# Optimization experiments

Measured on AMD Instinct MI355X. Metric: run time of the kernel, lower is better.

Reference implementation:

```python
import jax, jax.numpy as jnp
import numpy as np
from jax import lax

CONF_THR = 0.5
NMS_THR = 0.5
B, N, C = 2, 8192, 80


def setup_inputs() -> dict:
    key = jax.random.key(0)
    k1, k2, k3, k4 = jax.random.split(key, 4)
    cls_logits = jax.random.normal(k1, (B, N, C), dtype=jnp.float32)
    deltas = jax.random.normal(k2, (B, N, 4), dtype=jnp.float32) * 0.1
    # anchors: valid x1,y1,x2,y2 boxes in [0,1]
    ctr = jax.random.uniform(k3, (N, 2), minval=0.05, maxval=0.95)
    wh = jax.random.uniform(k4, (N, 2), minval=0.02, maxval=0.2)
    anchors = jnp.concatenate([ctr - 0.5 * wh, ctr + 0.5 * wh], axis=-1).astype(jnp.float32)
    return {"cls_logits": cls_logits, "deltas": deltas, "anchors": anchors}


def apply_deltas_to_anchors(deltas, anchors):
    aw = anchors[:, 2] - anchors[:, 0]
    ah = anchors[:, 3] - anchors[:, 1]
    acx = anchors[:, 0] + 0.5 * aw
    acy = anchors[:, 1] + 0.5 * ah
    dx, dy = deltas[..., 0], deltas[..., 1]
    dw = jnp.minimum(deltas[..., 2], 4.0)
    dh = jnp.minimum(deltas[..., 3], 4.0)
    pcx = dx * aw + acx
    pcy = dy * ah + acy
    pw = jnp.exp(dw) * aw
    ph = jnp.exp(dh) * ah
    boxes = jnp.stack([pcx - 0.5 * pw, pcy - 0.5 * ph,
                       pcx + 0.5 * pw, pcy + 0.5 * ph], axis=-1)
    return jnp.clip(boxes, 0.0, 1.0)


def iou_matrix(b):  # b: [N,4] -> [N,N]
    x1, y1, x2, y2 = b[:, 0], b[:, 1], b[:, 2], b[:, 3]
    area = (x2 - x1) * (y2 - y1)
    ix1 = jnp.maximum(x1[:, None], x1[None, :])
    iy1 = jnp.maximum(y1[:, None], y1[None, :])
    ix2 = jnp.minimum(x2[:, None], x2[None, :])
    iy2 = jnp.minimum(y2[:, None], y2[None, :])
    inter = jnp.clip(ix2 - ix1, 0.0) * jnp.clip(iy2 - iy1, 0.0)
    union = area[:, None] + area[None, :] - inter
    return inter / jnp.maximum(union, 1e-9)


def nms_keep(boxes, scores, valid, thr):
    """Greedy NMS; returns bool keep mask in original order (padded shape N)."""
    n = boxes.shape[0]
    order = jnp.argsort(-scores)
    bs = boxes[order]
    vs = valid[order]
    iou = iou_matrix(bs)  # [N,N] in score order
    idx = jnp.arange(n)

    def body(keep, i):
        suppressed = jnp.any((iou[i] > thr) & keep & (idx < i))
        k = vs[i] & ~suppressed
        keep = keep.at[i].set(k)
        return keep, None

    keep_sorted, _ = lax.scan(body, jnp.zeros(n, dtype=bool), idx)
    return jnp.zeros(n, dtype=bool).at[order].set(keep_sorted)


def reference(cls_logits, deltas, anchors):
    all_scores = jax.nn.sigmoid(cls_logits)                 # [B,N,C]
    boxes = apply_deltas_to_anchors(deltas, anchors)        # [B,N,4]
    max_scores = jnp.max(all_scores, axis=-1)               # [B,N]
    labels = jnp.argmax(all_scores, axis=-1)                # [B,N]
    conf_mask = max_scores > CONF_THR
    w = boxes[..., 2] - boxes[..., 0]
    h = boxes[..., 3] - boxes[..., 1]
    size_mask = (w > 0.01) & (h > 0.01) & (w < 0.99) & (h < 0.99)
    valid = conf_mask & size_mask
    keep = jax.vmap(nms_keep, in_axes=(0, 0, 0, None))(boxes, max_scores, valid, NMS_THR)
    # Padded (jit-friendly) equivalent of the ragged per-image outputs:
    return boxes, max_scores, labels, keep, all_scores
```

## Files before the change

kernel.cpp:

```cpp
#include <hip/hip_runtime.h>

constexpr int NB = 2;
constexpr int NN = 8192;
constexpr int NC = 80;
constexpr int ROWS = NN + 1;

constexpr size_t OFF_BOXES  = 0;
constexpr size_t OFF_SCORES = (size_t)NB * NN * 4;
constexpr size_t OFF_LABELS = OFF_SCORES + (size_t)NB * NN;
constexpr size_t OFF_KEEP   = OFF_LABELS + (size_t)NB * NN;
constexpr size_t OFF_ALL    = OFF_KEEP + (size_t)NB * NN;

constexpr size_t WS_KEYS  = 0;
constexpr size_t WS_VBYTE = WS_KEYS + (size_t)NB * NN * 8;
constexpr size_t WS_ORDER = WS_VBYTE + (size_t)NB * NN;
constexpr size_t WS_SBOX  = WS_ORDER + (size_t)NB * NN * 4;
constexpr size_t WS_VBITS = WS_SBOX + (size_t)NB * NN * 16;
constexpr size_t WS_MASK  = WS_VBITS + (size_t)NB * 128 * 8;
constexpr size_t WS_DNM   = WS_MASK + (size_t)NB * ROWS * 128 * 8;
constexpr size_t WS_PART  = WS_DNM + (size_t)NB * 128 * 4 * 64 * 8;
constexpr size_t WS_TOTAL = WS_PART + (size_t)NB * 8 * NN * 4;
constexpr size_t WS_TOTAL_OLD = WS_PART;
constexpr int ROW_CAP = 64;
constexpr size_t WS_RDEG = WS_TOTAL;
constexpr size_t WS_RENT = WS_RDEG + (size_t)NB * NN * 4;
constexpr size_t WS_OVF  = WS_RENT + (size_t)NB * NN * ROW_CAP * 2;
constexpr size_t WS_TOTAL_SPARSE = WS_OVF + 64;
constexpr int DNM_WORDS = NB * 128 * 4 * 64;
constexpr int NSEG = 8;

typedef unsigned long long u64;
typedef __attribute__((ext_vector_type(2))) unsigned long long u64x2;

__device__ inline void lbar() {
  __builtin_amdgcn_s_waitcnt(0xc07f);
  __builtin_amdgcn_s_barrier();
}

__device__ inline u64 readlane64(u64 v, int src) {
  unsigned int lo = (unsigned int)__builtin_amdgcn_readlane((int)(unsigned int)v, src);
  unsigned int hi = (unsigned int)__builtin_amdgcn_readlane((int)(unsigned int)(v >> 32), src);
  return ((u64)hi << 32) | lo;
}

__device__ inline u64 readfirstlane64(u64 v) {
  unsigned int lo = (unsigned int)__builtin_amdgcn_readfirstlane((int)(unsigned int)v);
  unsigned int hi = (unsigned int)__builtin_amdgcn_readfirstlane((int)(unsigned int)(v >> 32));
  return ((u64)hi << 32) | lo;
}

__device__ inline float iou_pair(const float4 p, const float4 q) {
#pragma clang fp contract(off)
  float areaA = (p.z - p.x) * (p.w - p.y);
  float areaB = (q.z - q.x) * (q.w - q.y);
  float ix1 = fmaxf(p.x, q.x);
  float iy1 = fmaxf(p.y, q.y);
  float ix2 = fminf(p.z, q.z);
  float iy2 = fminf(p.w, q.w);
  float inter = fmaxf(ix2 - ix1, 0.0f) * fmaxf(iy2 - iy1, 0.0f);
  float uni = areaA + areaB - inter;
  return inter / fmaxf(uni, 1e-9f);
}

__device__ inline float clip01(float v) { return fminf(fmaxf(v, 0.0f), 1.0f); }

__global__ __launch_bounds__(256) void decode_kernel(
    const float* __restrict__ logits, const float4* __restrict__ deltas,
    const float4* __restrict__ anchors, float4* __restrict__ boxes_out,
    float* __restrict__ scores_out, float* __restrict__ labels_out,
    float* __restrict__ all_out, u64* __restrict__ keys,
    unsigned char* __restrict__ vbyte, u64* __restrict__ vbits) {
#pragma clang fp contract(off)
  if (blockIdx.x == 0 && threadIdx.x < NB * 128) vbits[threadIdx.x] = 0ull;
  int wid = (blockIdx.x * 256 + threadIdx.x) >> 6;
  int lane = threadIdx.x & 63;
  int n = wid & (NN - 1);
  size_t base = (size_t)wid * NC;

  float x0 = logits[base + lane];
  float sig0 = 1.0f / (1.0f + expf(-x0));
  all_out[base + lane] = sig0;
  float bs = sig0;
  int bidx = lane;
  if (lane < NC - 64) {
    float x1 = logits[base + 64 + lane];
    float sig1 = 1.0f / (1.0f + expf(-x1));
    all_out[base + 64 + lane] = sig1;
    if (sig1 > bs) { bs = sig1; bidx = lane + 64; }
  }
  for (int off = 32; off; off >>= 1) {
    float os = __shfl_xor(bs, off, 64);
    int oi = __shfl_xor(bidx, off, 64);
    if (os > bs || (os == bs && oi < bidx)) { bs = os; bidx = oi; }
  }
  if (lane == 0) {
    float4 d = deltas[wid];
    float4 a = anchors[n];
    float aw = a.z - a.x, ah = a.w - a.y;
    float acx = a.x + 0.5f * aw, acy = a.y + 0.5f * ah;
    float dw = fminf(d.z, 4.0f), dh = fminf(d.w, 4.0f);
    float pcx = d.x * aw + acx;
    float pcy = d.y * ah + acy;
    float pw = expf(dw) * aw;
    float ph = expf(dh) * ah;
    float4 bx;
    bx.x = clip01(pcx - 0.5f * pw);
    bx.y = clip01(pcy - 0.5f * ph);
    bx.z = clip01(pcx + 0.5f * pw);
    bx.w = clip01(pcy + 0.5f * ph);
    boxes_out[wid] = bx;
    scores_out[wid] = bs;
    labels_out[wid] = (float)bidx;
    float bw = bx.z - bx.x, bh = bx.w - bx.y;
    bool valid = (bs > 0.5f) && (bw > 0.01f) && (bh > 0.01f) &&
                 (bw < 0.99f) && (bh < 0.99f);
    vbyte[wid] = valid ? 1 : 0;
    keys[wid] = ((u64)__float_as_uint(bs) << 32) | (unsigned int)(NN - 1 - n);
  }
}

__global__ __launch_bounds__(1024) void rank_part_kernel(
    const u64* __restrict__ keys, int* __restrict__ part,
    u64* __restrict__ dnm, unsigned int* rowdeg, unsigned int* ovf) {
  int b = blockIdx.z, seg = blockIdx.y, rb = blockIdx.x;
  int gid = ((blockIdx.z * NSEG + blockIdx.y) * gridDim.x + blockIdx.x) * 1024 +
            threadIdx.x;
  if (gid < DNM_WORDS) dnm[gid] = 0ull;
  if (rowdeg) {
    if (gid < NB * NN) rowdeg[gid] = 0u;
    if (gid < NB) ovf[gid] = 0u;
  }
  int r = threadIdx.x & 255;
  int q = threadIdx.x >> 8;
  int i = rb * 256 + r;
  const u64* kb = keys + (size_t)b * NN;
  u64 myk = kb[i];
  int cnt2 = 0;
  int j0 = seg * (NN / NSEG) + q * (NN / NSEG / 4);
  int j1 = j0 + NN / NSEG / 4;
#pragma unroll 8
  for (int j = j0; j < j1; ++j) {
    u64 kj = kb[j];
    cnt2 += (kj > myk) ? 1 : 0;
  }
  __shared__ unsigned short partl[4][256];
  partl[q][r] = (unsigned short)cnt2;
  __syncthreads();
  if (threadIdx.x < 256) {
    int s = partl[0][r] + partl[1][r] + partl[2][r] + partl[3][r];
    part[((size_t)b * NSEG + seg) * NN + i] = s;
  }
}

__global__ __launch_bounds__(256) void rank_final_kernel(
    const int* __restrict__ part, const float4* __restrict__ boxes,
    const unsigned char* __restrict__ vbyte, int* __restrict__ order,
    float4* __restrict__ sbox, u64* __restrict__ vbits) {
  int b = blockIdx.y;
  int i = blockIdx.x * 256 + threadIdx.x;
  const int* pb = part + (size_t)b * NSEG * NN + i;
  int rank = 0;
#pragma unroll
  for (int s = 0; s < NSEG; ++s) rank += pb[(size_t)s * NN];
  order[(size_t)b * NN + rank] = i;
  sbox[(size_t)b * NN + rank] = boxes[(size_t)b * NN + i];
  if (vbyte[(size_t)b * NN + i])
    atomicOr(&vbits[b * 128 + (rank >> 6)], 1ull << (rank & 63));
}

__global__ __launch_bounds__(1024) void rank_kernel(
    const u64* __restrict__ keys, const float4* __restrict__ boxes,
    const unsigned char* __restrict__ vbyte, int* __restrict__ order,
    float4* __restrict__ sbox, u64* __restrict__ vbits,
    u64* __restrict__ dnm) {
  int b = blockIdx.y;
  int gid = (blockIdx.y * gridDim.x + blockIdx.x) * 1024 + threadIdx.x;
  for (int z = gid; z < DNM_WORDS; z += 65536) dnm[z] = 0ull;
  int r = threadIdx.x & 255;
  int q = threadIdx.x >> 8;
  int i = blockIdx.x * 256 + r;
  const u64* kb = keys + (size_t)b * NN;
  u64 myk = kb[i];
  int cnt = 0;
  int j0 = q * (NN / 4), j1 = j0 + NN / 4;
#pragma unroll 8
  for (int j = j0; j < j1; ++j) {
    u64 kj = kb[j];
    cnt += (kj > myk) ? 1 : 0;
  }
  __shared__ unsigned short part[4][256];
  part[q][r] = (unsigned short)cnt;
  __syncthreads();
  if (threadIdx.x < 256) {
    int rank = part[0][r] + part[1][r] + part[2][r] + part[3][r];
    order[(size_t)b * NN + rank] = i;
    sbox[(size_t)b * NN + rank] = boxes[(size_t)b * NN + i];
    if (vbyte[(size_t)b * NN + i])
      atomicOr(&vbits[b * 128 + (rank >> 6)], 1ull << (rank & 63));
  }
}

__global__ __launch_bounds__(64) void build_kernel(
    const float4* __restrict__ sbox, u64* __restrict__ mask,
    u64* __restrict__ dnm, unsigned int* rowdeg,
    unsigned short* rowent, unsigned int* ovf) {
  int byq = blockIdx.y, bxq = blockIdx.x, b = blockIdx.z;
  int by, bx;
  if (bxq >= byq) {
    by = byq; bx = bxq;
  } else if (byq == 64) {
    return;
  } else {
    by = 128 - byq; bx = 127 - bxq;
  }
  int lane = threadIdx.x;
  __shared__ float4 cb[64];
  cb[lane] = sbox[(size_t)b * NN + bx * 64 + lane];
  __syncthreads();
  int i = by * 64 + lane;
  float4 rb = sbox[(size_t)b * NN + i];
  u64 word = 0;
  for (int jj = 0; jj < 64; ++jj)
    if (iou_pair(rb, cb[jj]) > 0.5f) word |= 1ull << jj;
  u64 ent;
  if (bx == by) {
    word &= ~(1ull << lane);
    u64 lmask = (1ull << lane) - 1ull;
    mask[((size_t)b * ROWS + i) * 128 + bx] = word & ~lmask;
    dnm[(((size_t)b * 128 + by) * 4 + 0) * 64 + lane] = word & lmask;
    ent = word & ~lmask;
  } else {
    mask[((size_t)b * ROWS + i) * 128 + bx] = word;
    int dq = bx - by;
    if (dq < 4) dnm[(((size_t)b * 128 + by) * 4 + dq) * 64 + lane] = word;
    ent = word;
  }
  if (rowdeg && ent) {
    int wcnt = __popcll(ent);
    unsigned base = atomicAdd(&rowdeg[(size_t)b * NN + i], (unsigned)wcnt);
    if (base + (unsigned)wcnt <= (unsigned)ROW_CAP) {
      unsigned short* dst = rowent + ((size_t)b * NN + i) * ROW_CAP + base;
      int k = 0;
      u64 t = ent;
      while (t) {
        int bit = __builtin_ctzll(t);
        dst[k++] = (unsigned short)(bx * 64 + bit);
        t &= t - 1;
      }
    } else {
      atomicOr(&ovf[b], 1u);
    }
  }
}

__global__ __launch_bounds__(64) void reduce_sparse(
    const u64* __restrict__ vbits, const u64* __restrict__ dnm,
    const unsigned int* __restrict__ rowdeg,
    const unsigned short* __restrict__ rowent,
    const unsigned int* __restrict__ ovf, u64* __restrict__ keepw) {
  int b = blockIdx.x, lane = threadIdx.x;
  if (ovf[b]) return;
  __shared__ u64 s_remv[128];
  __shared__ u64 s_keep[128];
  s_remv[2 * lane] = 0ull;
  s_remv[2 * lane + 1] = 0ull;
  u64 va = vbits[b * 128 + 2 * lane];
  u64 vb2 = vbits[b * 128 + 2 * lane + 1];
  const u64* dnb = dnm + (size_t)b * 128 * 4 * 64;
  const unsigned int* dgb = rowdeg + (size_t)b * NN;
  const unsigned short* reb = rowent + (size_t)b * NN * ROW_CAP;

  u64 dA = dnb[lane];
  unsigned gA = dgb[lane];
  const u64x2* pA = (const u64x2*)(reb + (size_t)lane * ROW_CAP);
  u64x2 eA0 = pA[0], eA1 = pA[1], eA2 = pA[2], eA3 = pA[3];
  u64 dB = dnb[4 * 64 + lane];
  unsigned gB = dgb[64 + lane];
  const u64x2* pB = (const u64x2*)(reb + (size_t)(64 + lane) * ROW_CAP);
  u64x2 eB0 = pB[0], eB1 = pB[1], eB2 = pB[2], eB3 = pB[3];
  u64 dC = 0, dD = 0;
  unsigned gC = 0, gD = 0;
  u64x2 eC0{}, eC1{}, eC2{}, eC3{}, eD0{}, eD1{}, eD2{}, eD3{};

  auto body = [&](int c, u64 dcur, unsigned gcur, u64x2 e0, u64x2 e1,
                  u64x2 e2, u64x2 e3, u64& dnw, unsigned& gnw, u64x2& n0,
                  u64x2& n1, u64x2& n2, u64x2& n3) {
    int cp = (c + 2 < 128) ? c + 2 : 127;
    dnw = dnb[(size_t)cp * 4 * 64 + lane];
    gnw = dgb[cp * 64 + lane];
    const u64x2* np = (const u64x2*)(reb + (size_t)(cp * 64 + lane) * ROW_CAP);
    n0 = np[0]; n1 = np[1]; n2 = np[2]; n3 = np[3];
    u64 rm = s_remv[c];
    u64 vbw = readlane64((c & 1) ? vb2 : va, c >> 1);
    u64 cand = readfirstlane64(vbw & ~rm);
    u64 kept = cand;
    while (true) {
      u64 sup = __ballot((dcur & kept) != 0ull);
      u64 nk = cand & ~sup;
      if (nk == kept) break;
      kept = nk;
    }
    bool isk = (kept >> lane) & 1;
    int deg = (int)gcur;
    if (isk && deg > 0) {
      int lim = deg < 32 ? deg : 32;
#pragma unroll
      for (int k = 0; k < 32; ++k) {
        if (k < lim) {
          u64 src = (k < 16)
                        ? ((k < 8) ? ((k < 4) ? e0[0] : e0[1])
                                   : ((k < 12) ? e1[0] : e1[1]))
                        : ((k < 24) ? ((k < 20) ? e2[0] : e2[1])
                                    : ((k < 28) ? e3[0] : e3[1]));
          int j = (int)((src >> ((k & 3) * 16)) & 0xFFFFull);
          atomicOr(&s_remv[j >> 6], 1ull << (j & 63));
        }
      }
      for (int k = 32; k < deg; ++k) {
        int j = reb[(size_t)(c * 64 + lane) * ROW_CAP + k];
        atomicOr(&s_remv[j >> 6], 1ull << (j & 63));
      }
    }
    if (lane == 0) s_keep[c] = kept;
  };

  for (int c = 0; c < 128; c += 4) {
    body(c + 0, dA, gA, eA0, eA1, eA2, eA3, dC, gC, eC0, eC1, eC2, eC3);
    body(c + 1, dB, gB, eB0, eB1, eB2, eB3, dD, gD, eD0, eD1, eD2, eD3);
    body(c + 2, dC, gC, eC0, eC1, eC2, eC3, dA, gA, eA0, eA1, eA2, eA3);
    body(c + 3, dD, gD, eD0, eD1, eD2, eD3, dB, gB, eB0, eB1, eB2, eB3);
  }

  keepw[b * 128 + 2 * lane] = s_keep[2 * lane];
  keepw[b * 128 + 2 * lane + 1] = s_keep[2 * lane + 1];
}

struct TSet {
  u64x2 t0, t1, t2, t3, t4, t5, t6, t7, t8, t9;
};

__global__ __launch_bounds__(512) void reduce_dense(
    u64* __restrict__ mask, const u64* __restrict__ vbits,
    const u64* __restrict__ dnm, const unsigned int* __restrict__ ovf,
    u64* __restrict__ keepw) {
  int b = blockIdx.x, tid = threadIdx.x;
  if (ovf && ovf[b] == 0) return;
  int lane = tid & 63, wave = tid >> 6;
  __shared__ u64 s_remv[128];
  __shared__ u64 s_keep[128];
  __shared__ int s_rowlist[2][80];
  u64* mbz = mask + (size_t)b * ROWS * 128;
  const u64* mb = mbz;
  const u64* dn = dnm + (size_t)b * 128 * 4 * 64;

  for (int w = tid; w < 128; w += 512) {
    s_remv[w] = 0ull;
    mbz[(size_t)NN * 128 + w] = 0ull;
  }
  if (tid < 160) s_rowlist[tid / 80][tid % 80] = NN;

  u64 va = 0, vb2 = 0;
  u64 dA = 0, nA = 0, mA = 0, oA = 0, dB = 0, nB = 0, mB = 0, oB = 0;
  u64 dC = 0, nC = 0, mC = 0, oC = 0, dD = 0, nD = 0, mD = 0, oD = 0;
  if (wave == 0) {
    va = vbits[b * 128 + 2 * lane];
    vb2 = vbits[b * 128 + 2 * lane + 1];
    const u64* r0 = dn + lane;
    dA = r0[0]; nA = r0[64]; mA = r0[128]; oA = r0[192];
    const u64* r1 = dn + 4 * 64 + lane;
    dB = r1[0]; nB = r1[64]; mB = r1[128]; oB = r1[192];
  }
  TSet U{}, V{};
  int w0i = 2 * lane;
  __syncthreads();

  auto serial_body = [&](int c, u64 dcur, u64 ncur, u64 mcur, u64 ocur,
                         u64& dnew, u64& nnew, u64& mnew, u64& onew) {
    int cp = (c + 2 < 128) ? (c + 2) : 127;
    const u64* rp = dn + (size_t)cp * 4 * 64 + lane;
    dnew = rp[0]; nnew = rp[64]; mnew = rp[128]; onew = rp[192];
    int par = c & 1;
    u64 rm = s_remv[c];
    u64 vbw = readlane64(par ? vb2 : va, c >> 1);
    u64 cand = readfirstlane64(vbw & ~rm);
    u64 kept = cand;
    while (true) {
      u64 sup = __ballot((dcur & kept) != 0ull);
      u64 nk = cand & ~sup;
      if (nk == kept) break;
      kept = nk;
    }
    bool isk = (kept >> lane) & 1;
    if (c + 1 < 128 && isk && ncur) atomicOr(&s_remv[c + 1], ncur);
    if (c + 2 < 128 && isk && mcur) atomicOr(&s_remv[c + 2], mcur);
    if (c + 3 < 128 && isk && ocur) atomicOr(&s_remv[c + 3], ocur);
    s_rowlist[par][lane] = NN;
    if (isk) {
      int pos = __popcll(kept & ((1ull << lane) - 1ull));
      s_rowlist[par][pos] = c * 64 + lane;
    }
    if (lane == 0) s_keep[c] = kept;
  };

  auto bg_body = [&](int c, TSet& T) {
    u64 ax = T.t0[0] | T.t1[0] | T.t2[0] | T.t3[0] | T.t4[0] | T.t5[0] |
             T.t6[0] | T.t7[0] | T.t8[0] | T.t9[0];
    u64 ay = T.t0[1] | T.t1[1] | T.t2[1] | T.t3[1] | T.t4[1] | T.t5[1] |
             T.t6[1] | T.t7[1] | T.t8[1] | T.t9[1];
    int sc = (c + 1) & ~1;
    int wx = sc + w0i, wy = wx + 1;
    if (wx > c && wx < 128 && ax) atomicOr(&s_remv[wx], ax);
    if (wy > c && wy < 128 && ay) atomicOr(&s_remv[wy], ay);
    const int* rl = s_rowlist[(c - 1) & 1];
    int base = wave - 1;
    int si = (c + 3) & ~1;
    int w = si + w0i;
    bool wok = w < 128;
    const u64* mw = mb + w;
    const u64* zp = mbz + (size_t)NN * 128;
    int r0 = rl[base], r1 = rl[base + 7], r2 = rl[base + 14],
        r3 = rl[base + 21], r4 = rl[base + 28], r5 = rl[base + 35],
        r6 = rl[base + 42], r7 = rl[base + 49], r8 = rl[base + 56],
        r9 = rl[base + 63];
    T.t0 = *(const u64x2*)((wok && r0 != NN) ? mw + (size_t)r0 * 128 : zp);
    T.t1 = *(const u64x2*)((wok && r1 != NN) ? mw + (size_t)r1 * 128 : zp);
    T.t2 = *(const u64x2*)((wok && r2 != NN) ? mw + (size_t)r2 * 128 : zp);
    T.t3 = *(const u64x2*)((wok && r3 != NN) ? mw + (size_t)r3 * 128 : zp);
    T.t4 = *(const u64x2*)((wok && r4 != NN) ? mw + (size_t)r4 * 128 : zp);
    T.t5 = *(const u64x2*)((wok && r5 != NN) ? mw + (size_t)r5 * 128 : zp);
    T.t6 = *(const u64x2*)((wok && r6 != NN) ? mw + (size_t)r6 * 128 : zp);
    T.t7 = *(const u64x2*)((wok && r7 != NN) ? mw + (size_t)r7 * 128 : zp);
    T.t8 = *(const u64x2*)((wok && r8 != NN) ? mw + (size_t)r8 * 128 : zp);
    T.t9 = *(const u64x2*)((wok && r9 != NN) ? mw + (size_t)r9 * 128 : zp);
  };

  for (int c = 0; c < 128; c += 4) {
    if (wave == 0) serial_body(c, dA, nA, mA, oA, dC, nC, mC, oC);
    else bg_body(c, U);
    lbar();
    if (wave == 0) serial_body(c + 1, dB, nB, mB, oB, dD, nD, mD, oD);
    else bg_body(c + 1, V);
    lbar();
    if (wave == 0) serial_body(c + 2, dC, nC, mC, oC, dA, nA, mA, oA);
    else bg_body(c + 2, U);
    lbar();
    if (wave == 0) serial_body(c + 3, dD, nD, mD, oD, dB, nB, mB, oB);
    else bg_body(c + 3, V);
    lbar();
  }

  __syncthreads();
  for (int w = tid; w < 128; w += 512) keepw[b * 128 + w] = s_keep[w];
}

__global__ __launch_bounds__(256) void scatter_keep(
    const u64* __restrict__ keepw, const int* __restrict__ order,
    float* __restrict__ keep_out) {
  int b = blockIdx.y;
  int p = blockIdx.x * 256 + threadIdx.x;
  int orig = order[(size_t)b * NN + p];
  keep_out[(size_t)b * NN + orig] =
      ((keepw[b * 128 + (p >> 6)] >> (p & 63)) & 1) ? 1.0f : 0.0f;
}

__global__ __launch_bounds__(1024) void nms_fallback(
    const float4* __restrict__ sbox, const u64* __restrict__ vbits,
    const int* __restrict__ order, float* __restrict__ keep_out) {
  int b = blockIdx.x, tid = threadIdx.x;
  __shared__ u64 dead[128];
  __shared__ int s_next;
  __shared__ float4 s_box;
  for (int w = tid; w < 128; w += 1024) dead[w] = ~vbits[b * 128 + w];
  for (int p = tid; p < NN; p += 1024)
    keep_out[(size_t)b * NN + order[(size_t)b * NN + p]] = 0.0f;
  __syncthreads();
  int i = 0;
  while (true) {
    if (tid == 0) {
      int nxt = NN;
      int w = i >> 6;
      u64 live = ~dead[w] & (~0ull << (i & 63));
      while (true) {
        if (live) { nxt = w * 64 + __builtin_ctzll(live); break; }
        if (++w >= 128) break;
        live = ~dead[w];
      }
      s_next = nxt;
      if (nxt < NN) {
        s_box = sbox[(size_t)b * NN + nxt];
        keep_out[(size_t)b * NN + order[(size_t)b * NN + nxt]] = 1.0f;
      }
    }
    __syncthreads();
    i = s_next;
    if (i >= NN) break;
    float4 kb = s_box;
    for (int j = i + 1 + tid; j < NN; j += 1024) {
      if (iou_pair(kb, sbox[(size_t)b * NN + j]) > 0.5f)
        atomicOr(&dead[j >> 6], 1ull << (j & 63));
    }
    __syncthreads();
    i = i + 1;
  }
}

extern "C" void kernel_launch(void* const* d_in, const int* in_sizes, int n_in,
                              void* d_out, int out_size, void* d_ws, size_t ws_size,
                              hipStream_t stream) {
  const float* logits = (const float*)d_in[0];
  const float4* deltas = (const float4*)d_in[1];
  const float4* anchors = (const float4*)d_in[2];
  float* out = (float*)d_out;
  float4* boxes_out = (float4*)(out + OFF_BOXES);
  float* scores_out = out + OFF_SCORES;
  float* labels_out = out + OFF_LABELS;
  float* keep_out = out + OFF_KEEP;
  float* all_out = out + OFF_ALL;

  char* ws = (char*)d_ws;
  u64* keys = (u64*)(ws + WS_KEYS);
  unsigned char* vbyte = (unsigned char*)(ws + WS_VBYTE);
  int* order = (int*)(ws + WS_ORDER);
  float4* sbox = (float4*)(ws + WS_SBOX);
  u64* vbits = (u64*)(ws + WS_VBITS);
  u64* mask = (u64*)(ws + WS_MASK);
  u64* dnm = (u64*)(ws + WS_DNM);
  int* part = (int*)(ws + WS_PART);
  unsigned int* rowdeg = (unsigned int*)(ws + WS_RDEG);
  unsigned short* rowent = (unsigned short*)(ws + WS_RENT);
  unsigned int* ovf = (unsigned int*)(ws + WS_OVF);
  u64* keepw = (u64*)(ws + WS_KEYS);

  decode_kernel<<<dim3(NB * NN / 4), dim3(256), 0, stream>>>(
      logits, deltas, anchors, boxes_out, scores_out, labels_out, all_out,
      keys, vbyte, vbits);
  if (ws_size >= WS_TOTAL_SPARSE) {
    rank_part_kernel<<<dim3(NN / 256, NSEG, NB), dim3(1024), 0, stream>>>(
        keys, part, dnm, rowdeg, ovf);
    rank_final_kernel<<<dim3(NN / 256, NB), dim3(256), 0, stream>>>(
        part, (const float4*)boxes_out, vbyte, order, sbox, vbits);
    build_kernel<<<dim3(128, 65, NB), dim3(64), 0, stream>>>(
        sbox, mask, dnm, rowdeg, rowent, ovf);
    reduce_sparse<<<dim3(NB), dim3(64), 0, stream>>>(vbits, dnm, rowdeg,
                                                     rowent, ovf, keepw);
    reduce_dense<<<dim3(NB), dim3(512), 0, stream>>>(mask, vbits, dnm, ovf,
                                                     keepw);
    scatter_keep<<<dim3(NN / 256, NB), dim3(256), 0, stream>>>(keepw, order,
                                                               keep_out);
  } else if (ws_size >= WS_TOTAL) {
    rank_part_kernel<<<dim3(NN / 256, NSEG, NB), dim3(1024), 0, stream>>>(
        keys, part, dnm, nullptr, nullptr);
    rank_final_kernel<<<dim3(NN / 256, NB), dim3(256), 0, stream>>>(
        part, (const float4*)boxes_out, vbyte, order, sbox, vbits);
    build_kernel<<<dim3(128, 65, NB), dim3(64), 0, stream>>>(
        sbox, mask, dnm, nullptr, nullptr, nullptr);
    reduce_dense<<<dim3(NB), dim3(512), 0, stream>>>(mask, vbits, dnm, nullptr,
                                                     keepw);
    scatter_keep<<<dim3(NN / 256, NB), dim3(256), 0, stream>>>(keepw, order,
                                                               keep_out);
  } else if (ws_size >= WS_TOTAL_OLD) {
    rank_kernel<<<dim3(NN / 256, NB), dim3(1024), 0, stream>>>(
        keys, (const float4*)boxes_out, vbyte, order, sbox, vbits, dnm);
    build_kernel<<<dim3(128, 65, NB), dim3(64), 0, stream>>>(
        sbox, mask, dnm, nullptr, nullptr, nullptr);
    reduce_dense<<<dim3(NB), dim3(512), 0, stream>>>(mask, vbits, dnm, nullptr,
                                                     keepw);
    scatter_keep<<<dim3(NN / 256, NB), dim3(256), 0, stream>>>(keepw, order,
                                                               keep_out);
  } else {
    rank_kernel<<<dim3(NN / 256, NB), dim3(1024), 0, stream>>>(
        keys, (const float4*)boxes_out, vbyte, order, sbox, vbits, dnm);
    nms_fallback<<<dim3(NB), dim3(1024), 0, stream>>>(sbox, vbits, order,
                                                      keep_out);
  }
}
```

Before: 274.8 us.

## Split sparse NMS reduce into producer wave prefetching rows via LDS ring

The sparse reduction kernel now runs two waves: one wave prefetches diagonal masks, degrees and the first 16 neighbour entries for upcoming 64-row chunks into a 4-slot shared-memory ring, while the other wave does the serial greedy suppression. The consumer's unrolled neighbour loop shrinks from 32 to 16 inline entries, is bounded by the wave-wide maximum degree, and falls back to global reads only when a kept row has more neighbours. This aims to take global-load latency off the serial chain, at the cost of a block barrier on every one of the 128 iterations.

```diff
diff --git a/kernel.cpp b/kernel.cpp
--- a/kernel.cpp
+++ b/kernel.cpp
@@ -253,86 +253,148 @@
   }
 }
 
-__global__ __launch_bounds__(64) void reduce_sparse(
+__global__ __launch_bounds__(128) void reduce_sparse(
     const u64* __restrict__ vbits, const u64* __restrict__ dnm,
     const unsigned int* __restrict__ rowdeg,
     const unsigned short* __restrict__ rowent,
     const unsigned int* __restrict__ ovf, u64* __restrict__ keepw) {
-  int b = blockIdx.x, lane = threadIdx.x;
+  int b = blockIdx.x, tid = threadIdx.x;
   if (ovf[b]) return;
+  int lane = tid & 63, wave = tid >> 6;
   __shared__ u64 s_remv[128];
   __shared__ u64 s_keep[128];
-  s_remv[2 * lane] = 0ull;
-  s_remv[2 * lane + 1] = 0ull;
-  u64 va = vbits[b * 128 + 2 * lane];
-  u64 vb2 = vbits[b * 128 + 2 * lane + 1];
+  __shared__ u64 s_diag[4][64];
+  __shared__ unsigned s_deg[4][64];
+  __shared__ u64 s_e0[4][64], s_e1[4][64], s_e2[4][64], s_e3[4][64];
+
   const u64* dnb = dnm + (size_t)b * 128 * 4 * 64;
-  const unsigned int* dgb = rowdeg + (size_t)b * NN;
+  const unsigned* dgb = rowdeg + (size_t)b * NN;
   const unsigned short* reb = rowent + (size_t)b * NN * ROW_CAP;
 
-  u64 dA = dnb[lane];
-  unsigned gA = dgb[lane];
-  const u64x2* pA = (const u64x2*)(reb + (size_t)lane * ROW_CAP);
-  u64x2 eA0 = pA[0], eA1 = pA[1], eA2 = pA[2], eA3 = pA[3];
-  u64 dB = dnb[4 * 64 + lane];
-  unsigned gB = dgb[64 + lane];
-  const u64x2* pB = (const u64x2*)(reb + (size_t)(64 + lane) * ROW_CAP);
-  u64x2 eB0 = pB[0], eB1 = pB[1], eB2 = pB[2], eB3 = pB[3];
-  u64 dC = 0, dD = 0;
-  unsigned gC = 0, gD = 0;
-  u64x2 eC0{}, eC1{}, eC2{}, eC3{}, eD0{}, eD1{}, eD2{}, eD3{};
-
-  auto body = [&](int c, u64 dcur, unsigned gcur, u64x2 e0, u64x2 e1,
-                  u64x2 e2, u64x2 e3, u64& dnw, unsigned& gnw, u64x2& n0,
-                  u64x2& n1, u64x2& n2, u64x2& n3) {
-    int cp = (c + 2 < 128) ? c + 2 : 127;
-    dnw = dnb[(size_t)cp * 4 * 64 + lane];
-    gnw = dgb[cp * 64 + lane];
-    const u64x2* np = (const u64x2*)(reb + (size_t)(cp * 64 + lane) * ROW_CAP);
-    n0 = np[0]; n1 = np[1]; n2 = np[2]; n3 = np[3];
-    u64 rm = s_remv[c];
-    u64 vbw = readlane64((c & 1) ? vb2 : va, c >> 1);
-    u64 cand = readfirstlane64(vbw & ~rm);
-    u64 kept = cand;
-    while (true) {
-      u64 sup = __ballot((dcur & kept) != 0ull);
-      u64 nk = cand & ~sup;
-      if (nk == kept) break;
-      kept = nk;
-    }
-    bool isk = (kept >> lane) & 1;
-    int deg = (int)gcur;
-    if (isk && deg > 0) {
-      int lim = deg < 32 ? deg : 32;
-#pragma unroll
-      for (int k = 0; k < 32; ++k) {
+  u64 va = 0, vb2 = 0;
+  u64 dA = 0, dB = 0;
+  unsigned gA = 0, gB = 0;
+  u64x2 eA0{}, eA1{}, eB0{}, eB1{};
+  if (wave == 0) {
+    s_remv[2 * lane] = 0ull;
+    s_remv[2 * lane + 1] = 0ull;
+    va = vbits[b * 128 + 2 * lane];
+    vb2 = vbits[b * 128 + 2 * lane + 1];
+  } else {
+    for (int cc = 0; cc < 3; ++cc) {
+      int row = cc * 64 + lane;
+      u64 d = dnb[(size_t)cc * 256 + lane];
+      unsigned g = dgb[row];
+      const u64x2* p = (const u64x2*)(reb + (size_t)row * ROW_CAP);
+      u64x2 e0 = p[0], e1 = p[1];
+      s_diag[cc][lane] = d;
+      s_deg[cc][lane] = g;
+      s_e0[cc][lane] = e0[0];
+      s_e1[cc][lane] = e0[1];
+      s_e2[cc][lane] = e1[0];
+      s_e3[cc][lane] = e1[1];
+    }
+    {
+      int row = 3 * 64 + lane;
+      dA = dnb[(size_t)3 * 256 + lane];
+      gA = dgb[row];
+      const u64x2* p = (const u64x2*)(reb + (size_t)row * ROW_CAP);
+      eA0 = p[0];
+      eA1 = p[1];
+    }
+    {
+      int row = 4 * 64 + lane;
+      dB = dnb[(size_t)4 * 256 + lane];
+      gB = dgb[row];
+      const u64x2* p = (const u64x2*)(reb + (size_t)row * ROW_CAP);
+      eB0 = p[0];
+      eB1 = p[1];
+    }
+  }
+  lbar();
+
+  for (int c = 0; c < 128; ++c) {
+    if (wave == 1) {
+      if (c + 3 < 128) {
+        int slot = (c + 3) & 3;
+        if (c & 1) {
+          s_diag[slot][lane] = dB;
+          s_deg[slot][lane] = gB;
+          s_e0[slot][lane] = eB0[0];
+          s_e1[slot][lane] = eB0[1];
+          s_e2[slot][lane] = eB1[0];
+          s_e3[slot][lane] = eB1[1];
+        } else {
+          s_diag[slot][lane] = dA;
+          s_deg[slot][lane] = gA;
+          s_e0[slot][lane] = eA0[0];
+          s_e1[slot][lane] = eA0[1];
+          s_e2[slot][lane] = eA1[0];
+          s_e3[slot][lane] = eA1[1];
+        }
+      }
+      int cp = (c + 5 < 128) ? c + 5 : 127;
+      int row = cp * 64 + lane;
+      const u64x2* p = (const u64x2*)(reb + (size_t)row * ROW_CAP);
+      if (c & 1) {
+        dB = dnb[(size_t)cp * 256 + lane];
+        gB = dgb[row];
+        eB0 = p[0];
+        eB1 = p[1];
+      } else {
+        dA = dnb[(size_t)cp * 256 + lane];
+        gA = dgb[row];
+        eA0 = p[0];
+        eA1 = p[1];
+      }
+    } else {
+      int slot = c & 3;
+      u64 dcur = s_diag[slot][lane];
+      unsigned deg = s_deg[slot][lane];
+      u64 q0 = s_e0[slot][lane], q1 = s_e1[slot][lane];
+      u64 q2 = s_e2[slot][lane], q3 = s_e3[slot][lane];
+      u64 rm = s_remv[c];
+      u64 vbw = readlane64((c & 1) ? vb2 : va, c >> 1);
+      u64 cand = readfirstlane64(vbw & ~rm);
+      u64 kept = cand;
+      while (true) {
+        u64 sup = __ballot((dcur & kept) != 0ull);
+        u64 nk = cand & ~sup;
+        if (nk == kept) break;
+        kept = nk;
+      }
+      bool isk = (kept >> lane) & 1;
+      int lim = (isk && deg) ? ((int)deg < 16 ? (int)deg : 16) : 0;
+      int wmax = lim;
+      for (int off = 32; off; off >>= 1) {
+        int t = __shfl_xor(wmax, off, 64);
+        wmax = t > wmax ? t : wmax;
+      }
+      for (int k = 0; k < wmax; ++k) {
         if (k < lim) {
-          u64 src = (k < 16)
-                        ? ((k < 8) ? ((k < 4) ? e0[0] : e0[1])
-                                   : ((k < 12) ? e1[0] : e1[1]))
-                        : ((k < 24) ? ((k < 20) ? e2[0] : e2[1])
-                                    : ((k < 28) ? e3[0] : e3[1]));
+          u64 src = (k < 8) ? (k < 4 ? q0 : q1) : (k < 12 ? q2 : q3);
           int j = (int)((src >> ((k & 3) * 16)) & 0xFFFFull);
           atomicOr(&s_remv[j >> 6], 1ull << (j & 63));
         }
       }
-      for (int k = 32; k < deg; ++k) {
-        int j = reb[(size_t)(c * 64 + lane) * ROW_CAP + k];
-        atomicOr(&s_remv[j >> 6], 1ull << (j & 63));
-      }
-    }
-    if (lane == 0) s_keep[c] = kept;
-  };
-
-  for (int c = 0; c < 128; c += 4) {
-    body(c + 0, dA, gA, eA0, eA1, eA2, eA3, dC, gC, eC0, eC1, eC2, eC3);
-    body(c + 1, dB, gB, eB0, eB1, eB2, eB3, dD, gD, eD0, eD1, eD2, eD3);
-    body(c + 2, dC, gC, eC0, eC1, eC2, eC3, dA, gA, eA0, eA1, eA2, eA3);
-    body(c + 3, dD, gD, eD0, eD1, eD2, eD3, dB, gB, eB0, eB1, eB2, eB3);
-  }
-
-  keepw[b * 128 + 2 * lane] = s_keep[2 * lane];
-  keepw[b * 128 + 2 * lane + 1] = s_keep[2 * lane + 1];
+      if (__ballot(isk && (int)deg > 16)) {
+        if (isk && (int)deg > 16) {
+          const unsigned short* rp = reb + (size_t)(c * 64 + lane) * ROW_CAP;
+          for (int k = 16; k < (int)deg; ++k) {
+            int j = rp[k];
+            atomicOr(&s_remv[j >> 6], 1ull << (j & 63));
+          }
+        }
+      }
+      if (lane == 0) s_keep[c] = kept;
+    }
+    lbar();
+  }
+
+  if (wave == 0) {
+    keepw[b * 128 + 2 * lane] = s_keep[2 * lane];
+    keepw[b * 128 + 2 * lane + 1] = s_keep[2 * lane + 1];
+  }
 }
 
 struct TSet {
@@ -541,8 +603,8 @@
         part, (const float4*)boxes_out, vbyte, order, sbox, vbits);
     build_kernel<<<dim3(128, 65, NB), dim3(64), 0, stream>>>(
         sbox, mask, dnm, rowdeg, rowent, ovf);
-    reduce_sparse<<<dim3(NB), dim3(64), 0, stream>>>(vbits, dnm, rowdeg,
-                                                     rowent, ovf, keepw);
+    reduce_sparse<<<dim3(NB), dim3(128), 0, stream>>>(vbits, dnm, rowdeg,
+                                                      rowent, ovf, keepw);
     reduce_dense<<<dim3(NB), dim3(512), 0, stream>>>(mask, vbits, dnm, ovf,
                                                      keepw);
     scatter_keep<<<dim3(NN / 256, NB), dim3(256), 0, stream>>>(keepw, order,
```

Result: slower. 287.1 us (+4.5%).
